# Performance work log

Hardware: AMD Instinct MI355X
Metric: run time of the kernel (lower is better)

Reference implementation:

```python
import jax, jax.numpy as jnp
import numpy as np

EMBED = 512
HEADS = 1
HEAD_DIM = EMBED // HEADS  # 512 (heads must be 1 for the original torch code to run)
N, S = 4, 4096


def setup_inputs() -> dict:
    key = jax.random.key(0)
    ks = jax.random.split(key, 9)
    scale = 1.0 / np.sqrt(EMBED)
    return {
        "values": jax.random.normal(ks[0], (N, 1, S, EMBED), dtype=jnp.float32),
        "keys": jax.random.normal(ks[1], (N, 1, S, EMBED), dtype=jnp.float32),
        "query": jax.random.normal(ks[2], (N, 1, S, EMBED), dtype=jnp.float32),
        "mask": jax.random.randint(ks[3], (N, 1, S, S), 0, 2, dtype=jnp.int32),
        "Wv": jax.random.normal(ks[4], (EMBED, EMBED), dtype=jnp.float32) * scale,
        "Wk": jax.random.normal(ks[5], (EMBED, EMBED), dtype=jnp.float32) * scale,
        "Wq": jax.random.normal(ks[6], (EMBED, EMBED), dtype=jnp.float32) * scale,
        "Wo": jax.random.normal(ks[7], (EMBED, EMBED), dtype=jnp.float32) * scale,
        "bo": jnp.zeros((EMBED,), dtype=jnp.float32),
    }


def reference(values, keys, query, mask, Wv, Wk, Wq, Wo, bo):
    n = query.shape[0]
    q_len = query.shape[2]
    # reshape(N, -1, heads, head_dim); inputs are [N, 1, S, E] -> [N, S, H, Dh]
    v = values.reshape(n, -1, HEADS, HEAD_DIM)
    k = keys.reshape(n, -1, HEADS, HEAD_DIM)
    q = query.reshape(n, -1, HEADS, HEAD_DIM)
    # per-module linear projections (nn.Linear: y = x @ W.T)
    v = jnp.einsum('nlhd,ed->nlhe', v, Wv)
    k = jnp.einsum('nlhd,ed->nlhe', k, Wk)
    q = jnp.einsum('nqhd,ed->nqhe', q, Wq)
    # full [N, H, Q, K] score matrix, as in the original
    energy = jnp.einsum('nqhd,nkhd->nhqk', q, k)
    energy = jnp.where(mask == 0, jnp.float32(-1e20), energy)
    attn = jax.nn.softmax(energy / np.sqrt(HEAD_DIM), axis=3)
    out = jnp.einsum('nhql,nlhd->nqhd', attn, v).reshape(n, q_len, HEADS * HEAD_DIM)
    return out @ Wo.T + bo
```

## Files before the change

### kernel.cpp

```cpp
#include <hip/hip_runtime.h>

typedef __bf16 bf16x8 __attribute__((ext_vector_type(8)));
typedef __bf16 bf16x4 __attribute__((ext_vector_type(4)));
typedef float f32x4 __attribute__((ext_vector_type(4)));
typedef float f32x16 __attribute__((ext_vector_type(16)));

#define MFMA16(a, b, c) __builtin_amdgcn_mfma_f32_16x16x32_bf16((a), (b), (c), 0, 0, 0)
#define MFMA32(a, b, c) __builtin_amdgcn_mfma_f32_32x32x16_bf16((a), (b), (c), 0, 0, 0)

static constexpr int SEQ = 4096;
static constexpr int DIM = 512;

typedef __attribute__((address_space(3))) void lds_void;
typedef __attribute__((address_space(1))) const void gbl_void;

__device__ __forceinline__ void glds16(const void* g, void* l) {
    __builtin_amdgcn_global_load_lds((gbl_void*)g, (lds_void*)l, 16, 0, 0);
}

__device__ __forceinline__ bf16x8 cvt8f(const float* __restrict__ p) {
    float4 f0 = *(const float4*)p;
    float4 f1 = *(const float4*)(p + 4);
    bf16x8 v;
    v[0] = (__bf16)f0.x; v[1] = (__bf16)f0.y; v[2] = (__bf16)f0.z; v[3] = (__bf16)f0.w;
    v[4] = (__bf16)f1.x; v[5] = (__bf16)f1.y; v[6] = (__bf16)f1.z; v[7] = (__bf16)f1.w;
    return v;
}

__global__ __launch_bounds__(256)
void convert_w(const float* __restrict__ wq, const float* __restrict__ wk,
               const float* __restrict__ wv, const float* __restrict__ wo,
               __bf16* __restrict__ out)
{
    const int z = blockIdx.y;
    const float* src = (z == 0) ? wq : (z == 1) ? wk : (z == 2) ? wv : wo;
    __bf16* dst = out + (size_t)z * DIM * DIM;
    const int i = (blockIdx.x * 256 + threadIdx.x) * 8;
    *(bf16x8*)(dst + i) = cvt8f(src + i);
}

__global__ __launch_bounds__(256, 3)
void gemm_qkv(const float* __restrict__ Aq, const float* __restrict__ Ak,
              const float* __restrict__ Av, const __bf16* __restrict__ Wb,
              __bf16* __restrict__ Qp, __bf16* __restrict__ Kp,
              __bf16* __restrict__ Vtp)
{
    const int z = blockIdx.z;
    const float* Ap = (z == 0) ? Aq : (z == 1) ? Ak : Av;
    const __bf16* Bp = Wb + (size_t)z * DIM * DIM;
    __bf16* Cp = (z == 0) ? Qp : (z == 1) ? Kp : Vtp;

    __shared__ __align__(16) char smem[128 * 132 * 2];
    __bf16* As = (__bf16*)smem;
    __bf16* Bs = (__bf16*)(smem + 16384);

    const int tid  = threadIdx.x;
    const int wave = tid >> 6;
    const int lane = tid & 63;
    const int quad = lane >> 4;
    const int l16  = lane & 15;
    const int m0 = blockIdx.x * 128;
    const int n0 = blockIdx.y * 128;
    const int wm = (wave >> 1) * 64;
    const int wn = (wave & 1) * 64;

    f32x4 acc[4][4] = {};

    for (int k0 = 0; k0 < DIM; k0 += 64) {
        #pragma unroll
        for (int i = 0; i < 4; i++) {
            const int j = wave * 4 + i;
            const int t = j * 64 + lane;
            const int row = t >> 3, c8 = t & 7;
            glds16(Bp + (size_t)(n0 + row) * DIM + k0 + c8 * 8, &Bs[j * 512]);
            *(bf16x8*)&As[t * 8] =
                cvt8f(Ap + (size_t)(m0 + row) * DIM + k0 + c8 * 8);
        }
        __syncthreads();
        #pragma unroll
        for (int kk = 0; kk < 2; kk++) {
            bf16x8 af[4], bg[4];
            #pragma unroll
            for (int mt = 0; mt < 4; mt++)
                af[mt] = *(const bf16x8*)&As[(wm + mt * 16 + l16) * 64 + kk * 32 + quad * 8];
            #pragma unroll
            for (int nt = 0; nt < 4; nt++)
                bg[nt] = *(const bf16x8*)&Bs[(wn + nt * 16 + l16) * 64 + kk * 32 + quad * 8];
            #pragma unroll
            for (int mt = 0; mt < 4; mt++)
                #pragma unroll
                for (int nt = 0; nt < 4; nt++)
                    acc[mt][nt] = MFMA16(af[mt], bg[nt], acc[mt][nt]);
        }
        __syncthreads();
    }

    if (z < 2) {
        #pragma unroll
        for (int mt = 0; mt < 4; mt++)
            #pragma unroll
            for (int nt = 0; nt < 4; nt++)
                #pragma unroll
                for (int r = 0; r < 4; r++)
                    Cp[(size_t)(m0 + wm + mt * 16 + quad * 4 + r) * DIM
                       + n0 + wn + nt * 16 + l16] = (__bf16)acc[mt][nt][r];
    } else {
        __bf16* Tt = (__bf16*)smem;
        __syncthreads();
        #pragma unroll
        for (int mt = 0; mt < 4; mt++)
            #pragma unroll
            for (int nt = 0; nt < 4; nt++)
                #pragma unroll
                for (int r = 0; r < 4; r++)
                    Tt[(wm + mt * 16 + quad * 4 + r) * 132 + wn + nt * 16 + l16]
                        = (__bf16)acc[mt][nt][r];
        __syncthreads();
        const int nb  = m0 >> 12;
        const int s0m = m0 & 4095;
        const int d   = tid >> 1;
        const int sh  = (tid & 1) * 64;
        __bf16* dst = Cp + (size_t)nb * DIM * SEQ + (size_t)(n0 + d) * SEQ + s0m + sh;
        #pragma unroll
        for (int i = 0; i < 8; i++) {
            bf16x8 vv;
            #pragma unroll
            for (int e = 0; e < 8; e++) vv[e] = Tt[(sh + i * 8 + e) * 132 + d];
            *(bf16x8*)(dst + i * 8) = vv;
        }
    }
}

__global__ __launch_bounds__(256, 3)
void gemm_out(const __bf16* __restrict__ Ap, const __bf16* __restrict__ Bp,
              float* __restrict__ Cp, const float* __restrict__ bias)
{
    __shared__ __align__(16) __bf16 As[128 * 64];
    __shared__ __align__(16) __bf16 Bs[128 * 64];
    const int tid  = threadIdx.x;
    const int wave = tid >> 6;
    const int lane = tid & 63;
    const int quad = lane >> 4;
    const int l16  = lane & 15;
    const int m0 = blockIdx.x * 128;
    const int n0 = blockIdx.y * 128;
    const int wm = (wave >> 1) * 64;
    const int wn = (wave & 1) * 64;

    f32x4 acc[4][4] = {};

    for (int k0 = 0; k0 < DIM; k0 += 64) {
        #pragma unroll
        for (int i = 0; i < 4; i++) {
            const int j = wave * 4 + i;
            const int c = j * 64 + lane;
            const int row = c >> 3, c8 = c & 7;
            glds16(Ap + (size_t)(m0 + row) * DIM + k0 + c8 * 8, &As[j * 512]);
            glds16(Bp + (size_t)(n0 + row) * DIM + k0 + c8 * 8, &Bs[j * 512]);
        }
        __syncthreads();
        #pragma unroll
        for (int kk = 0; kk < 2; kk++) {
            bf16x8 af[4], bg[4];
            #pragma unroll
            for (int mt = 0; mt < 4; mt++)
                af[mt] = *(const bf16x8*)&As[(wm + mt * 16 + l16) * 64 + kk * 32 + quad * 8];
            #pragma unroll
            for (int nt = 0; nt < 4; nt++)
                bg[nt] = *(const bf16x8*)&Bs[(wn + nt * 16 + l16) * 64 + kk * 32 + quad * 8];
            #pragma unroll
            for (int mt = 0; mt < 4; mt++)
                #pragma unroll
                for (int nt = 0; nt < 4; nt++)
                    acc[mt][nt] = MFMA16(af[mt], bg[nt], acc[mt][nt]);
        }
        __syncthreads();
    }
    #pragma unroll
    for (int mt = 0; mt < 4; mt++)
        #pragma unroll
        for (int nt = 0; nt < 4; nt++)
            #pragma unroll
            for (int r = 0; r < 4; r++) {
                const int col = n0 + wn + nt * 16 + l16;
                Cp[(size_t)(m0 + wm + mt * 16 + quad * 4 + r) * DIM + col]
                    = acc[mt][nt][r] + bias[col];
            }
}

#define MKC(v, r4) ((r4) == 0 ? (v).x : (r4) == 1 ? (v).y : (r4) == 2 ? (v).z : (v).w)

__global__ __launch_bounds__(512, 1)
void flash_attn(__bf16* __restrict__ Qp, const __bf16* __restrict__ Kp,
                const __bf16* __restrict__ Vt, const int* __restrict__ mask)
{
    constexpr float SCALE = 0.044194173824159216f;

    __shared__ __bf16 KQ[2][20480];
    __shared__ __bf16 P[64 * 256];
    __shared__ float pmax[8 * 66];
    __shared__ float psum[8 * 66];

    const int bid  = blockIdx.x;
    const int n    = bid & 3;
    const int q0   = (bid >> 2) * 64;
    const int tid  = threadIdx.x;
    const int w    = tid >> 6;
    const int lane = tid & 63;
    const int l32  = lane & 31;
    const int half = lane >> 5;
    const int r8   = lane >> 3;
    const int c8   = lane & 7;
    const int gc   = c8 ^ r8;

    const __bf16* Qb = Qp + (size_t)n * SEQ * DIM;
    const __bf16* Kb = Kp + (size_t)n * SEQ * DIM;
    const __bf16* Vb = Vt + (size_t)n * DIM * SEQ;
    const int*    Mb = mask + (size_t)n * SEQ * SEQ;
    __bf16*       AO = Qp + (size_t)n * SEQ * DIM;

    auto stageK = [&](int slot, int k0, int dc) {
        #pragma unroll
        for (int i = 0; i < 4; i++) {
            const int R = (i * 8 + w) * 8 + r8;
            glds16(Kb + (size_t)(k0 + R) * DIM + dc * 64 + gc * 8,
                   &KQ[slot][(i * 8 + w) * 512]);
        }
    };
    auto stageV = [&](int slot, int k0, int vc) {
        const int h = vc >> 2, kc2 = vc & 3;
        #pragma unroll
        for (int i = 0; i < 4; i++) {
            const int R = (i * 8 + w) * 8 + r8;
            glds16(Vb + (size_t)(h * 256 + R) * SEQ + k0 + kc2 * 64 + gc * 8,
                   &KQ[slot][(i * 8 + w) * 512]);
        }
    };
    auto stageQ = [&](int slot, int dc) {
        glds16(Qb + (size_t)(q0 + w * 8 + r8) * DIM + dc * 64 + gc * 8,
               &KQ[slot][16384 + w * 512]);
    };

    float m0 = -__builtin_inff(), m1 = -__builtin_inff();
    float l0 = 0.f, l1 = 0.f;
    f32x16 o00 = {}, o01 = {}, o10 = {}, o11 = {};

    stageK(0, 0, 0);
    stageQ(0, 0);
    __syncthreads();
    int cur = 0;

    #pragma unroll 1
    for (int j = 0; j < 16; j++) {
        const int k0 = j * 256;

        int4 mk0[4], mk1[4];
        {
            const int* mp0 = Mb + (size_t)(q0 + l32) * SEQ + k0 + 32 * w + 4 * half;
            const int* mp1 = mp0 + (size_t)32 * SEQ;
            #pragma unroll
            for (int g = 0; g < 4; g++) {
                mk0[g] = *(const int4*)(mp0 + 8 * g);
                mk1[g] = *(const int4*)(mp1 + 8 * g);
            }
        }

        f32x16 s0 = {}, s1 = {};
        #pragma unroll 1
        for (int dc = 0; dc < 8; dc++) {
            const int nxt = cur ^ 1;
            if (dc < 7) { stageK(nxt, k0, dc + 1); stageQ(nxt, dc + 1); }
            else        { stageV(nxt, k0, 0); }
            const __bf16* Kc = KQ[cur];
            const __bf16* Qc = KQ[cur] + 16384;
            __builtin_amdgcn_s_setprio(1);
            #pragma unroll
            for (int ks = 0; ks < 4; ks++) {
                const int ch = (2 * ks + half) ^ (l32 & 7);
                bf16x8 a  = *(const bf16x8*)&Kc[(32 * w + l32) * 64 + ch * 8];
                bf16x8 b0 = *(const bf16x8*)&Qc[l32 * 64 + ch * 8];
                bf16x8 b1 = *(const bf16x8*)&Qc[(32 + l32) * 64 + ch * 8];
                s0 = MFMA32(a, b0, s0);
                s1 = MFMA32(a, b1, s1);
            }
            __builtin_amdgcn_s_setprio(0);
            if (dc == 7) {
                float mx0 = s0[0], mx1 = s1[0];
                #pragma unroll
                for (int r = 1; r < 16; r++) { mx0 = fmaxf(mx0, s0[r]); mx1 = fmaxf(mx1, s1[r]); }
                mx0 = fmaxf(mx0, __shfl_xor(mx0, 32));
                mx1 = fmaxf(mx1, __shfl_xor(mx1, 32));
                if (half == 0) pmax[w * 66 + l32]      = mx0;
                else           pmax[w * 66 + 32 + l32] = mx1;
            }
            __syncthreads();
            cur = nxt;
        }

        float mp0v = pmax[l32], mp1v = pmax[32 + l32];
        #pragma unroll
        for (int w2 = 1; w2 < 8; w2++) {
            mp0v = fmaxf(mp0v, pmax[w2 * 66 + l32]);
            mp1v = fmaxf(mp1v, pmax[w2 * 66 + 32 + l32]);
        }
        const float mn0 = fmaxf(m0, mp0v * SCALE);
        const float mn1 = fmaxf(m1, mp1v * SCALE);
        const float a0 = __expf(m0 - mn0);
        const float a1 = __expf(m1 - mn1);
        m0 = mn0; m1 = mn1;
        #pragma unroll
        for (int r = 0; r < 16; r++) {
            o00[r] *= a0; o10[r] *= a0;
            o01[r] *= a1; o11[r] *= a1;
        }

        float ls0 = 0.f, ls1 = 0.f;
        #pragma unroll
        for (int g = 0; g < 4; g++) {
            bf16x4 pv0, pv1;
            #pragma unroll
            for (int r4 = 0; r4 < 4; r4++) {
                const int r = g * 4 + r4;
                float p0 = __expf(s0[r] * SCALE - mn0);
                float p1 = __expf(s1[r] * SCALE - mn1);
                p0 = MKC(mk0[g], r4) ? p0 : 0.f;
                p1 = MKC(mk1[g], r4) ? p1 : 0.f;
                ls0 += p0; ls1 += p1;
                pv0[r4] = (__bf16)p0;
                pv1[r4] = (__bf16)p1;
            }
            const int c  = 4 * w + g;
            const int cp = (c & 24) | ((c & 7) ^ (l32 & 7));
            *(bf16x4*)&P[l32 * 256 + cp * 8 + 4 * half]        = pv0;
            *(bf16x4*)&P[(32 + l32) * 256 + cp * 8 + 4 * half] = pv1;
        }
        ls0 += __shfl_xor(ls0, 32);
        ls1 += __shfl_xor(ls1, 32);
        if (half == 0) psum[w * 66 + l32]      = ls0;
        else           psum[w * 66 + 32 + l32] = ls1;
        __syncthreads();

        {
            float ss0 = 0.f, ss1 = 0.f;
            #pragma unroll
            for (int w2 = 0; w2 < 8; w2++) {
                ss0 += psum[w2 * 66 + l32];
                ss1 += psum[w2 * 66 + 32 + l32];
            }
            l0 = l0 * a0 + ss0;
            l1 = l1 * a1 + ss1;
        }

        #pragma unroll 1
        for (int vc = 0; vc < 8; vc++) {
            const int nxt = cur ^ 1;
            if (vc < 7)       stageV(nxt, k0, vc + 1);
            else if (j < 15) { stageK(nxt, k0 + 256, 0); stageQ(nxt, 0); }
            const __bf16* Vc = KQ[cur];
            const int kc2 = vc & 3;
            __builtin_amdgcn_s_setprio(1);
            #pragma unroll
            for (int ks = 0; ks < 4; ks++) {
                const int ca = (2 * ks + half) ^ (l32 & 7);
                bf16x8 a = *(const bf16x8*)&Vc[(32 * w + l32) * 64 + ca * 8];
                const int ck = kc2 * 8 + 2 * ks + half;
                const int cp = (ck & 24) | ((ck & 7) ^ (l32 & 7));
                bf16x8 b0 = *(const bf16x8*)&P[l32 * 256 + cp * 8];
                bf16x8 b1 = *(const bf16x8*)&P[(32 + l32) * 256 + cp * 8];
                if (vc < 4) { o00 = MFMA32(a, b0, o00); o01 = MFMA32(a, b1, o01); }
                else        { o10 = MFMA32(a, b0, o10); o11 = MFMA32(a, b1, o11); }
            }
            __builtin_amdgcn_s_setprio(0);
            __syncthreads();
            cur = nxt;
        }
    }

    const float li0 = 1.f / l0, li1 = 1.f / l1;
    __bf16* ao0 = AO + (size_t)(q0 + l32) * DIM;
    __bf16* ao1 = AO + (size_t)(q0 + 32 + l32) * DIM;
    #pragma unroll
    for (int h = 0; h < 2; h++) {
        #pragma unroll
        for (int g = 0; g < 4; g++) {
            bf16x4 v00, v01;
            #pragma unroll
            for (int r4 = 0; r4 < 4; r4++) {
                const int r = g * 4 + r4;
                v00[r4] = (__bf16)((h ? o10[r] : o00[r]) * li0);
                v01[r4] = (__bf16)((h ? o11[r] : o01[r]) * li1);
            }
            const int d = h * 256 + 32 * w + g * 8 + 4 * half;
            *(bf16x4*)&ao0[d] = v00;
            *(bf16x4*)&ao1[d] = v01;
        }
    }
}

extern "C" void kernel_launch(void* const* d_in, const int* in_sizes, int n_in,
                              void* d_out, int out_size, void* d_ws, size_t ws_size,
                              hipStream_t stream)
{
    const float* values = (const float*)d_in[0];
    const float* keys   = (const float*)d_in[1];
    const float* query  = (const float*)d_in[2];
    const int*   mask   = (const int*)d_in[3];
    const float* Wv = (const float*)d_in[4];
    const float* Wk = (const float*)d_in[5];
    const float* Wq = (const float*)d_in[6];
    const float* Wo = (const float*)d_in[7];
    const float* bo = (const float*)d_in[8];
    float* out = (float*)d_out;

    char* ws = (char*)d_ws;
    __bf16* Qp  = (__bf16*)(ws);
    __bf16* Kp  = (__bf16*)(ws + (16u << 20));
    __bf16* Vt  = (__bf16*)(ws + (32u << 20));
    __bf16* wbf = (__bf16*)(ws + (48u << 20));

    const int M = 4 * SEQ;

    convert_w<<<dim3(128, 4), 256, 0, stream>>>(Wq, Wk, Wv, Wo, wbf);

    gemm_qkv<<<dim3(M / 128, DIM / 128, 3), 256, 0, stream>>>(
        query, keys, values, wbf, Qp, Kp, Vt);

    flash_attn<<<256, 512, 0, stream>>>(Qp, Kp, Vt, mask);

    gemm_out<<<dim3(M / 128, DIM / 128), 256, 0, stream>>>(
        Qp , wbf + 3 * DIM * DIM, out, bo);
}
```

Baseline: 727.3 us.

## Load K/V fragments directly to registers and keep Q resident in LDS

Drops the LDS double-buffered staging of K, V and Q chunks along with the per-chunk __syncthreads. Q for the block's 64 rows now sits in LDS once, stored with a padded, swizzled layout. K and V MFMA operands are loaded straight from global memory into registers, software-pipelined one chunk ahead, and barriers are cut to a few per key tile using raw s_waitcnt/s_barrier. This trades LDS traffic and barrier stalls for register pressure and uncoalesced per-lane global loads that can expose memory latency.

```diff
diff --git a/kernel.cpp b/kernel.cpp
--- a/kernel.cpp
+++ b/kernel.cpp
@@ -189,14 +189,17 @@
 }
 
 #define MKC(v, r4) ((r4) == 0 ? (v).x : (r4) == 1 ? (v).y : (r4) == 2 ? (v).z : (v).w)
+#define WAITLGKM() asm volatile("s_waitcnt lgkmcnt(0)" ::: "memory")
+#define BARRIER()  asm volatile("s_barrier" ::: "memory")
 
 __global__ __launch_bounds__(512, 1)
 void flash_attn(__bf16* __restrict__ Qp, const __bf16* __restrict__ Kp,
                 const __bf16* __restrict__ Vt, const int* __restrict__ mask)
 {
     constexpr float SCALE = 0.044194173824159216f;
-
-    __shared__ __bf16 KQ[2][20480];
+    constexpr int QPITCH = 520;
+
+    __shared__ __bf16 Qs[64 * QPITCH];
     __shared__ __bf16 P[64 * 256];
     __shared__ float pmax[8 * 66];
     __shared__ float psum[8 * 66];
@@ -209,9 +212,6 @@
     const int lane = tid & 63;
     const int l32  = lane & 31;
     const int half = lane >> 5;
-    const int r8   = lane >> 3;
-    const int c8   = lane & 7;
-    const int gc   = c8 ^ r8;
 
     const __bf16* Qb = Qp + (size_t)n * SEQ * DIM;
     const __bf16* Kb = Kp + (size_t)n * SEQ * DIM;
@@ -219,36 +219,67 @@
     const int*    Mb = mask + (size_t)n * SEQ * SEQ;
     __bf16*       AO = Qp + (size_t)n * SEQ * DIM;
 
-    auto stageK = [&](int slot, int k0, int dc) {
-        #pragma unroll
-        for (int i = 0; i < 4; i++) {
-            const int R = (i * 8 + w) * 8 + r8;
-            glds16(Kb + (size_t)(k0 + R) * DIM + dc * 64 + gc * 8,
-                   &KQ[slot][(i * 8 + w) * 512]);
-        }
-    };
-    auto stageV = [&](int slot, int k0, int vc) {
-        const int h = vc >> 2, kc2 = vc & 3;
-        #pragma unroll
-        for (int i = 0; i < 4; i++) {
-            const int R = (i * 8 + w) * 8 + r8;
-            glds16(Vb + (size_t)(h * 256 + R) * SEQ + k0 + kc2 * 64 + gc * 8,
-                   &KQ[slot][(i * 8 + w) * 512]);
-        }
-    };
-    auto stageQ = [&](int slot, int dc) {
-        glds16(Qb + (size_t)(q0 + w * 8 + r8) * DIM + dc * 64 + gc * 8,
-               &KQ[slot][16384 + w * 512]);
-    };
+    #pragma unroll
+    for (int i = 0; i < 8; i++) {
+        const int r  = i * 8 + w;
+        const int hr = (r & 7) ^ ((r >> 3) & 7);
+        const int cs = (lane & 56) | ((lane & 7) ^ hr);
+        glds16(Qb + (size_t)(q0 + r) * DIM + cs * 8, &Qs[r * QPITCH]);
+    }
+
+    const __bf16* kPtr  = Kb + (size_t)(32 * w + l32) * DIM + half * 8;
+    const __bf16* vPtr0 = Vb + (size_t)(32 * w + l32) * SEQ + half * 8;
+    const __bf16* vPtr1 = vPtr0 + (size_t)256 * SEQ;
+
+    const int h0 = (l32 & 7) ^ ((l32 >> 3) & 7);
+    const int h1 = h0 ^ 4;
+    int q0off[4], q1off[4];
+    #pragma unroll
+    for (int ks = 0; ks < 4; ks++) {
+        q0off[ks] = ((2 * ks + half) ^ h0) * 8;
+        q1off[ks] = ((2 * ks + half) ^ h1) * 8;
+    }
+    const int qrow0 = l32 * QPITCH;
+    const int qrow1 = (32 + l32) * QPITCH;
 
     float m0 = -__builtin_inff(), m1 = -__builtin_inff();
     float l0 = 0.f, l1 = 0.f;
     f32x16 o00 = {}, o01 = {}, o10 = {}, o11 = {};
-
-    stageK(0, 0, 0);
-    stageQ(0, 0);
+    f32x16 s0, s1;
+
+    bf16x8 kA[4], kB[4], vA[4], vB[4];
+
+#define LOADK(buf, dc_) { _Pragma("unroll") \
+    for (int ks = 0; ks < 4; ks++) \
+        buf[ks] = *(const bf16x8*)(kPtr + (dc_) * 64 + ks * 16); }
+
+#define LOADV(buf, vc_) { const __bf16* vp_ = ((vc_) < 4) ? vPtr0 : vPtr1; \
+    _Pragma("unroll") \
+    for (int ks = 0; ks < 4; ks++) \
+        buf[ks] = *(const bf16x8*)(vp_ + ((vc_) & 3) * 64 + ks * 16); }
+
+#define QK8(buf, dc_) { __builtin_amdgcn_s_setprio(1); \
+    _Pragma("unroll") \
+    for (int ks = 0; ks < 4; ks++) { \
+        bf16x8 b0 = *(const bf16x8*)&Qs[qrow0 + (dc_) * 64 + q0off[ks]]; \
+        bf16x8 b1 = *(const bf16x8*)&Qs[qrow1 + (dc_) * 64 + q1off[ks]]; \
+        s0 = MFMA32(buf[ks], b0, s0); \
+        s1 = MFMA32(buf[ks], b1, s1); \
+    } __builtin_amdgcn_s_setprio(0); }
+
+#define PV8(buf, vc_) { __builtin_amdgcn_s_setprio(1); \
+    _Pragma("unroll") \
+    for (int ks = 0; ks < 4; ks++) { \
+        const int ck = ((vc_) & 3) * 8 + 2 * ks + half; \
+        const int cp = (ck & 24) | ((ck & 7) ^ (l32 & 7)); \
+        bf16x8 b0 = *(const bf16x8*)&P[l32 * 256 + cp * 8]; \
+        bf16x8 b1 = *(const bf16x8*)&P[(32 + l32) * 256 + cp * 8]; \
+        if ((vc_) < 4) { o00 = MFMA32(buf[ks], b0, o00); o01 = MFMA32(buf[ks], b1, o01); } \
+        else           { o10 = MFMA32(buf[ks], b0, o10); o11 = MFMA32(buf[ks], b1, o11); } \
+    } __builtin_amdgcn_s_setprio(0); }
+
     __syncthreads();
-    int cur = 0;
+    LOADK(kA, 0);
 
     #pragma unroll 1
     for (int j = 0; j < 16; j++) {
@@ -265,37 +296,29 @@
             }
         }
 
-        f32x16 s0 = {}, s1 = {};
-        #pragma unroll 1
-        for (int dc = 0; dc < 8; dc++) {
-            const int nxt = cur ^ 1;
-            if (dc < 7) { stageK(nxt, k0, dc + 1); stageQ(nxt, dc + 1); }
-            else        { stageV(nxt, k0, 0); }
-            const __bf16* Kc = KQ[cur];
-            const __bf16* Qc = KQ[cur] + 16384;
-            __builtin_amdgcn_s_setprio(1);
-            #pragma unroll
-            for (int ks = 0; ks < 4; ks++) {
-                const int ch = (2 * ks + half) ^ (l32 & 7);
-                bf16x8 a  = *(const bf16x8*)&Kc[(32 * w + l32) * 64 + ch * 8];
-                bf16x8 b0 = *(const bf16x8*)&Qc[l32 * 64 + ch * 8];
-                bf16x8 b1 = *(const bf16x8*)&Qc[(32 + l32) * 64 + ch * 8];
-                s0 = MFMA32(a, b0, s0);
-                s1 = MFMA32(a, b1, s1);
-            }
-            __builtin_amdgcn_s_setprio(0);
-            if (dc == 7) {
-                float mx0 = s0[0], mx1 = s1[0];
-                #pragma unroll
-                for (int r = 1; r < 16; r++) { mx0 = fmaxf(mx0, s0[r]); mx1 = fmaxf(mx1, s1[r]); }
-                mx0 = fmaxf(mx0, __shfl_xor(mx0, 32));
-                mx1 = fmaxf(mx1, __shfl_xor(mx1, 32));
-                if (half == 0) pmax[w * 66 + l32]      = mx0;
-                else           pmax[w * 66 + 32 + l32] = mx1;
-            }
-            __syncthreads();
-            cur = nxt;
-        }
+        s0 = (f32x16){}; s1 = (f32x16){};
+        LOADK(kB, 1); QK8(kA, 0);
+        LOADK(kA, 2); QK8(kB, 1);
+        LOADK(kB, 3); QK8(kA, 2);
+        LOADK(kA, 4); QK8(kB, 3);
+        LOADK(kB, 5); QK8(kA, 4);
+        LOADK(kA, 6); QK8(kB, 5);
+        LOADK(kB, 7); QK8(kA, 6);
+                      QK8(kB, 7);
+
+        {
+            float mx0 = s0[0], mx1 = s1[0];
+            #pragma unroll
+            for (int r = 1; r < 16; r++) { mx0 = fmaxf(mx0, s0[r]); mx1 = fmaxf(mx1, s1[r]); }
+            mx0 = fmaxf(mx0, __shfl_xor(mx0, 32));
+            mx1 = fmaxf(mx1, __shfl_xor(mx1, 32));
+            if (half == 0) pmax[w * 66 + l32]      = mx0;
+            else           pmax[w * 66 + 32 + l32] = mx1;
+        }
+        WAITLGKM();
+        BARRIER();
+
+        LOADV(vA, 0);
 
         float mp0v = pmax[l32], mp1v = pmax[32 + l32];
         #pragma unroll
@@ -338,7 +361,8 @@
         ls1 += __shfl_xor(ls1, 32);
         if (half == 0) psum[w * 66 + l32]      = ls0;
         else           psum[w * 66 + 32 + l32] = ls1;
-        __syncthreads();
+        WAITLGKM();
+        BARRIER();
 
         {
             float ss0 = 0.f, ss1 = 0.f;
@@ -351,29 +375,21 @@
             l1 = l1 * a1 + ss1;
         }
 
-        #pragma unroll 1
-        for (int vc = 0; vc < 8; vc++) {
-            const int nxt = cur ^ 1;
-            if (vc < 7)       stageV(nxt, k0, vc + 1);
-            else if (j < 15) { stageK(nxt, k0 + 256, 0); stageQ(nxt, 0); }
-            const __bf16* Vc = KQ[cur];
-            const int kc2 = vc & 3;
-            __builtin_amdgcn_s_setprio(1);
-            #pragma unroll
-            for (int ks = 0; ks < 4; ks++) {
-                const int ca = (2 * ks + half) ^ (l32 & 7);
-                bf16x8 a = *(const bf16x8*)&Vc[(32 * w + l32) * 64 + ca * 8];
-                const int ck = kc2 * 8 + 2 * ks + half;
-                const int cp = (ck & 24) | ((ck & 7) ^ (l32 & 7));
-                bf16x8 b0 = *(const bf16x8*)&P[l32 * 256 + cp * 8];
-                bf16x8 b1 = *(const bf16x8*)&P[(32 + l32) * 256 + cp * 8];
-                if (vc < 4) { o00 = MFMA32(a, b0, o00); o01 = MFMA32(a, b1, o01); }
-                else        { o10 = MFMA32(a, b0, o10); o11 = MFMA32(a, b1, o11); }
-            }
-            __builtin_amdgcn_s_setprio(0);
-            __syncthreads();
-            cur = nxt;
-        }
+        LOADV(vB, 1); PV8(vA, 0);
+        LOADV(vA, 2); PV8(vB, 1);
+        LOADV(vB, 3); PV8(vA, 2);
+        LOADV(vA, 4); PV8(vB, 3);
+        LOADV(vB, 5); PV8(vA, 4);
+        LOADV(vA, 6); PV8(vB, 5);
+        LOADV(vB, 7); PV8(vA, 6);
+                      PV8(vB, 7);
+
+        kPtr  += 256 * DIM;
+        vPtr0 += 256;
+        vPtr1 += 256;
+        if (j < 15) LOADK(kA, 0);
+        WAITLGKM();
+        BARRIER();
     }
 
     const float li0 = 1.f / l0, li1 = 1.f / l1;
@@ -395,6 +411,10 @@
             *(bf16x4*)&ao1[d] = v01;
         }
     }
+#undef LOADK
+#undef LOADV
+#undef QK8
+#undef PV8
 }
 
 extern "C" void kernel_launch(void* const* d_in, const int* in_sizes, int n_in,
```

Result: no change. 728.1 us (+0.1%).
